# Optimization experiments

Measured on AMD Instinct MI355X. Metric: run time of the kernel, lower is better.

## Reference

```python
import jax, jax.numpy as jnp
import numpy as np

EPS = 1e-7
PI = np.pi


def _vel_to_R(vel):
    # vel: [..., 3] -> rotation matrix [..., 3, 3] (ZY convention from spherical angles)
    rho = jnp.linalg.norm(vel, axis=-1, keepdims=True)
    theta = jnp.arctan2(vel[..., 1:2], vel[..., 0:1])
    theta = theta + (theta < 0).astype(theta.dtype) * (2.0 * PI)  # symmetric_theta=False
    phi = jnp.arccos(jnp.clip(vel[..., 2:3] / (rho + EPS), -1.0, 1.0))
    ct, st = jnp.cos(theta)[..., 0], jnp.sin(theta)[..., 0]
    cp, sp = jnp.cos(phi)[..., 0], jnp.sin(phi)[..., 0]
    z = jnp.zeros_like(ct)
    R = jnp.stack([
        jnp.stack([cp * ct, -st, sp * ct], -1),
        jnp.stack([cp * st, ct, sp * st], -1),
        jnp.stack([-sp, z, cp], -1),
    ], -2)
    return R


def _rotate(R, x):
    return jnp.einsum('...ij,...j->...i', R, x)


def setup_inputs() -> dict:
    key = jax.random.key(0)
    B, N, H, D = 128, 100, 128, 3
    in_size = 2 * D  # 6
    nef = 3 * D + D * (D - 1) // 2 + in_size  # 18 edge features
    ks = jax.random.split(key, 12)

    inputs = jax.random.normal(ks[0], (B, N, in_size), jnp.float32)

    # fully connected edges (no self loops)
    send_np, recv_np = np.nonzero(~np.eye(N, dtype=bool))
    send_edges = jnp.asarray(send_np, jnp.int32)
    recv_edges = jnp.asarray(recv_np, jnp.int32)

    def lin(k, fin, fout):
        return jax.random.normal(k, (fin, fout), jnp.float32) / np.sqrt(fin)

    return dict(
        inputs=inputs,
        W1=lin(ks[1], nef, H), b1=jnp.zeros((H,), jnp.float32),
        W2=lin(ks[2], H, H), b2=jnp.zeros((H,), jnp.float32),
        Wr=lin(ks[3], in_size, H), br=jnp.zeros((H,), jnp.float32),
        W3=lin(ks[4], H, H), b3=jnp.zeros((H,), jnp.float32),
        W4=lin(ks[5], H, H), b4=jnp.zeros((H,), jnp.float32),
        W5=lin(ks[6], H, in_size), b5=jnp.zeros((in_size,), jnp.float32),
        send_edges=send_edges, recv_edges=recv_edges,
    )


def reference(inputs, W1, b1, W2, b2, Wr, br, W3, b3, W4, b4, W5, b5,
              send_edges, recv_edges):
    D = 3
    B, N, _ = inputs.shape

    # ---- Localizer.canonicalize_inputs ----
    vel = inputs[..., D:2 * D]
    Rnode = _vel_to_R(vel)                       # [B,N,3,3]
    Rinv_node = jnp.swapaxes(Rnode, -1, -2)
    canon_vel = _rotate(Rinv_node, vel)
    rel_feat = jnp.concatenate([jnp.zeros_like(canon_vel), canon_vel], -1)  # [B,N,6]

    # ---- Localizer.create_edge_attr ----
    x_j = inputs[:, send_edges]                  # [B,E,6] senders
    x_i = inputs[:, recv_edges]                  # [B,E,6] receivers
    R = _vel_to_R(x_i[..., D:2 * D])
    R_inv = jnp.swapaxes(R, -1, -2)
    rel_pos = x_j[..., :D] - x_i[..., :D]
    rot_rel = _rotate(R_inv, rel_pos)
    send_R = _vel_to_R(x_j[..., D:2 * D])
    rot_or = R_inv @ send_R
    euler = jnp.stack([
        jnp.arctan2(rot_or[..., 1, 0], rot_or[..., 0, 0]),
        jnp.arcsin(-rot_or[..., 2, 0]),
        jnp.arctan2(rot_or[..., 2, 1], rot_or[..., 2, 2]),
    ], -1) / PI
    dist = jnp.linalg.norm(rel_pos, axis=-1, keepdims=True)
    rho_e = jnp.linalg.norm(rot_rel, axis=-1, keepdims=True)
    theta_e = jnp.arctan2(rot_rel[..., 1:2], rot_rel[..., 0:1])  # symmetric theta
    phi_e = jnp.arccos(jnp.clip(rot_rel[..., 2:3] / (rho_e + EPS), -1.0, 1.0))
    rot_vel = _rotate(R_inv, x_j[..., D:2 * D])
    edge_attr = jnp.concatenate(
        [rot_rel, euler, dist, theta_e, phi_e, rot_vel], -1)   # [B,E,12]
    edge_attr = jnp.concatenate([edge_attr, rel_feat[:, recv_edges]], -1)  # [B,E,18]

    # ---- GNN: edge MLP + scatter-mean + out MLP (dropout off in eval) ----
    h = jax.nn.silu(edge_attr @ W1 + b1) @ W2 + b2               # [B,E,H]
    agg = jnp.zeros((B, N, h.shape[-1]), h.dtype).at[:, recv_edges].add(h)
    cnt = jnp.zeros((N,), h.dtype).at[recv_edges].add(1.0)
    agg = agg / jnp.maximum(cnt, 1.0)[None, :, None]             # scatter mean
    aug = agg + rel_feat @ Wr + br
    p = jax.nn.relu(aug @ W3 + b3)
    p = jax.nn.relu(p @ W4 + b4)
    pred = p @ W5 + b5                                           # [B,N,6]

    # ---- Globalizer: rotate each 3-vector chunk back to global frame ----
    gl = jnp.concatenate(
        [_rotate(Rnode, pred[..., i:i + D]) for i in range(0, pred.shape[-1], D)], -1)
    return inputs + gl
```

## Files before the change

kernel.cpp:

```cpp
#include <hip/hip_runtime.h>
#include <math.h>

#define EPSF 1e-7f
constexpr int NN  = 100;
constexpr int DEG = 99;
constexpr int IN  = 6;
constexpr int H   = 128;
constexpr int G   = 4;
constexpr float INV_PI = 0.3183098861837907f;

typedef __attribute__((ext_vector_type(4))) _Float16 half4;
typedef __attribute__((ext_vector_type(8))) _Float16 half8;
typedef __attribute__((ext_vector_type(4))) float f32x4;

constexpr int XST = 144;

__device__ __forceinline__ float clampf(float x, float lo, float hi) {
    return fminf(fmaxf(x, lo), hi);
}
__device__ __forceinline__ float fast_sig(float x) {
    return __builtin_amdgcn_rcpf(1.f + __expf(-x));
}
__device__ __forceinline__ float fast_atan2(float y, float x) {
    float ax = fabsf(x), ay = fabsf(y);
    float mx = fmaxf(ax, ay), mn = fminf(ax, ay);
    float r = mn * __builtin_amdgcn_rcpf(fmaxf(mx, 1e-35f));
    float r2 = r * r;
    float p = fmaf(r2, -0.01172120f, 0.05265332f);
    p = fmaf(r2, p, -0.11643287f);
    p = fmaf(r2, p, 0.19354346f);
    p = fmaf(r2, p, -0.33262347f);
    p = fmaf(r2, p, 0.99997726f);
    float t = r * p;
    t = (ay > ax) ? (1.5707963267948966f - t) : t;
    t = (x < 0.f) ? (3.14159265358979323f - t) : t;
    return copysignf(t, y);
}
__device__ __forceinline__ float fast_asin(float z) {
    return fast_atan2(z, sqrtf(fmaxf(0.f, (1.f - z) * (1.f + z))));
}
__device__ __forceinline__ float fast_acos(float z) {
    return fast_atan2(sqrtf(fmaxf(0.f, (1.f - z) * (1.f + z))), z);
}
__device__ __forceinline__ void vel_to_R(float vx, float vy, float vz, float* R) {
    float rho = sqrtf(vx * vx + vy * vy + vz * vz);
    float rxy = sqrtf(vx * vx + vy * vy);
    float inv = __builtin_amdgcn_rcpf(rxy);
    bool big = rxy > 1e-30f;
    float ct = big ? vx * inv : 1.f;
    float st = big ? vy * inv : 0.f;
    float cp = clampf(vz * __builtin_amdgcn_rcpf(rho + EPSF), -1.f, 1.f);
    float sp = sqrtf(fmaxf(0.f, 1.f - cp * cp));
    R[0] = cp * ct; R[1] = -st; R[2] = sp * ct;
    R[3] = cp * st; R[4] = ct;  R[5] = sp * st;
    R[6] = -sp;     R[7] = 0.f; R[8] = cp;
}

__global__ void conv_w(const float* __restrict__ W1, const float* __restrict__ W2,
                       const float* __restrict__ W3, const float* __restrict__ W4,
                       half4* __restrict__ w1f, half8* __restrict__ wmlp) {
    int t = blockIdx.x * blockDim.x + threadIdx.x;
    if (t >= 104 * 64) return;
    int L = t & 63, f = t >> 6;
    int m = L & 15, qd = L >> 4;
    if (f < 8) {
        int n = f * 16 + m;
        half4 v;
#pragma unroll
        for (int j = 0; j < 4; ++j) {
            int k = qd * 4 + j;
            v[j] = (k < 12) ? (_Float16)W1[k * H + n] : (_Float16)0.f;
        }
        w1f[f * 64 + L] = v;
    } else {
        int ff = f - 8;
        int layer = ff >> 5, rest = ff & 31;
        int kt = rest >> 3, nt = rest & 7;
        const float* W = (layer == 0) ? W2 : (layer == 1) ? W3 : W4;
        int n = nt * 16 + m;
        half8 v;
#pragma unroll
        for (int j = 0; j < 8; ++j)
            v[j] = (_Float16)W[(kt * 32 + qd * 8 + j) * H + n];
        wmlp[((layer * 4 + kt) * 8 + nt) * 64 + L] = v;
    }
}

__global__ __launch_bounds__(128, 6)
void locs_fused(const float* __restrict__ in,
                const float* __restrict__ W1, const float* __restrict__ b1,
                const float* __restrict__ b2,
                const float* __restrict__ Wr, const float* __restrict__ br,
                const float* __restrict__ b3, const float* __restrict__ b4,
                const float* __restrict__ W5, const float* __restrict__ b5,
                const half4* __restrict__ w1f, const half8* __restrict__ wmlp,
                float* __restrict__ out) {
    __shared__ half4 eaA[2 * 7 * 64];
    __shared__ float poolF[1104];
    __shared__ _Float16 xh[G * XST];

    float* baseF = poolF;
    float* xFp   = poolF + 512;
    float* rmFp  = poolF + 1040;
    float* pbF   = poolF;
    float* predF = poolF + 384;

    const int tid = threadIdx.x;
    const int L   = tid & 63;
    const int wv  = tid >> 6;
    const int q   = L >> 4;
    const int lm  = L & 15;
    const int bn0 = blockIdx.x * G;
    const int bB  = bn0 / NN;
    const int n0  = bn0 - bB * NN;

    {
        half4 z = {0, 0, 0, 0};
#pragma unroll
        for (int i = 0; i < 7; ++i) eaA[tid + i * 128] = z;
    }
    if (tid < G) {
        const float* xi = in + (bn0 + tid) * IN;
        float R[9];
        vel_to_R(xi[3], xi[4], xi[5], R);
#pragma unroll
        for (int k = 0; k < 9; ++k) rmFp[tid * 16 + k] = R[k];
        rmFp[tid * 16 + 9]  = R[0] * xi[3] + R[3] * xi[4] + R[6] * xi[5];
        rmFp[tid * 16 + 10] = R[1] * xi[3] + R[4] * xi[4] + R[7] * xi[5];
        rmFp[tid * 16 + 11] = R[2] * xi[3] + R[5] * xi[4] + R[8] * xi[5];
        rmFp[tid * 16 + 12] = xi[0];
        rmFp[tid * 16 + 13] = xi[1];
        rmFp[tid * 16 + 14] = xi[2];
    }
    __syncthreads();

    {
        float w15 = W1[15 * H + tid], w16 = W1[16 * H + tid], w17 = W1[17 * H + tid];
        float b1c = b1[tid];
#pragma unroll
        for (int g = 0; g < G; ++g)
            baseF[g * 128 + tid] = b1c + rmFp[g * 16 + 9] * w15
                                 + rmFp[g * 16 + 10] * w16 + rmFp[g * 16 + 11] * w17;
    }
    half4 bfr[4];
#pragma unroll
    for (int i = 0; i < 4; ++i) bfr[i] = w1f[(wv * 4 + i) * 64 + L];

    auto edge_features = [&](int g, int buf) {
        if (tid < DEG) {
            int nG = n0 + g;
            int s = tid < nG ? tid : tid + 1;
            float Rn[9];
#pragma unroll
            for (int k = 0; k < 9; ++k) Rn[k] = rmFp[g * 16 + k];
            float pix = rmFp[g * 16 + 12], piy = rmFp[g * 16 + 13], piz = rmFp[g * 16 + 14];
            const float* xj = in + (bB * NN + s) * IN;
            float rel0 = xj[0] - pix, rel1 = xj[1] - piy, rel2 = xj[2] - piz;
            float vjx = xj[3], vjy = xj[4], vjz = xj[5];
            float Rs[9];
            vel_to_R(vjx, vjy, vjz, Rs);
            float rr0 = Rn[0] * rel0 + Rn[3] * rel1 + Rn[6] * rel2;
            float rr1 = Rn[1] * rel0 + Rn[4] * rel1 + Rn[7] * rel2;
            float rr2 = Rn[2] * rel0 + Rn[5] * rel1 + Rn[8] * rel2;
            float ro00 = Rn[0] * Rs[0] + Rn[3] * Rs[3] + Rn[6] * Rs[6];
            float ro10 = Rn[1] * Rs[0] + Rn[4] * Rs[3] + Rn[7] * Rs[6];
            float ro20 = Rn[2] * Rs[0] + Rn[5] * Rs[3] + Rn[8] * Rs[6];
            float ro21 = Rn[2] * Rs[1] + Rn[5] * Rs[4] + Rn[8] * Rs[7];
            float ro22 = Rn[2] * Rs[2] + Rn[5] * Rs[5] + Rn[8] * Rs[8];
            float dist = sqrtf(rel0 * rel0 + rel1 * rel1 + rel2 * rel2);
            half4 f0, f1, f2;
            f0[0] = (_Float16)rr0; f0[1] = (_Float16)rr1; f0[2] = (_Float16)rr2;
            f0[3] = (_Float16)(fast_atan2(ro10, ro00) * INV_PI);
            f1[0] = (_Float16)(fast_asin(clampf(-ro20, -1.f, 1.f)) * INV_PI);
            f1[1] = (_Float16)(fast_atan2(ro21, ro22) * INV_PI);
            f1[2] = (_Float16)dist;
            f1[3] = (_Float16)fast_atan2(rr1, rr0);
            f2[0] = (_Float16)fast_acos(clampf(rr2 * __builtin_amdgcn_rcpf(dist + EPSF), -1.f, 1.f));
            f2[1] = (_Float16)(Rn[0] * vjx + Rn[3] * vjy + Rn[6] * vjz);
            f2[2] = (_Float16)(Rn[1] * vjx + Rn[4] * vjy + Rn[7] * vjz);
            f2[3] = (_Float16)(Rn[2] * vjx + Rn[5] * vjy + Rn[8] * vjz);
            int t = tid >> 4, m = tid & 15;
            half4* dst = eaA + buf * 448 + t * 64;
            dst[m]      = f0;
            dst[16 + m] = f1;
            dst[32 + m] = f2;
        }
    };

    edge_features(0, 0);
    __syncthreads();

#pragma unroll
    for (int g = 0; g < G; ++g) {
        float part[4] = {0.f, 0.f, 0.f, 0.f};
        f32x4 c0, c1, c2, c3;
        {
            float bs0 = baseF[g * 128 + wv * 64 +  0 + lm];
            float bs1 = baseF[g * 128 + wv * 64 + 16 + lm];
            float bs2 = baseF[g * 128 + wv * 64 + 32 + lm];
            float bs3 = baseF[g * 128 + wv * 64 + 48 + lm];
            c0 = (f32x4){bs0, bs0, bs0, bs0};
            c1 = (f32x4){bs1, bs1, bs1, bs1};
            c2 = (f32x4){bs2, bs2, bs2, bs2};
            c3 = (f32x4){bs3, bs3, bs3, bs3};
        }
        const half4* ea = eaA + (g & 1) * 448;
#pragma unroll
        for (int t = 0; t < 6; ++t) {
            half4 a = ea[t * 64 + L];
            f32x4 d0 = __builtin_amdgcn_mfma_f32_16x16x16f16(a, bfr[0], c0, 0, 0, 0);
            f32x4 d1 = __builtin_amdgcn_mfma_f32_16x16x16f16(a, bfr[1], c1, 0, 0, 0);
            f32x4 d2 = __builtin_amdgcn_mfma_f32_16x16x16f16(a, bfr[2], c2, 0, 0, 0);
            f32x4 d3 = __builtin_amdgcn_mfma_f32_16x16x16f16(a, bfr[3], c3, 0, 0, 0);
#pragma unroll
            for (int r = 0; r < 4; ++r) {
                part[0] += d0[r] * fast_sig(d0[r]);
                part[1] += d1[r] * fast_sig(d1[r]);
                part[2] += d2[r] * fast_sig(d2[r]);
                part[3] += d3[r] * fast_sig(d3[r]);
            }
        }
        {
            half4 a = ea[6 * 64 + L];
            f32x4 d0 = __builtin_amdgcn_mfma_f32_16x16x16f16(a, bfr[0], c0, 0, 0, 0);
            f32x4 d1 = __builtin_amdgcn_mfma_f32_16x16x16f16(a, bfr[1], c1, 0, 0, 0);
            f32x4 d2 = __builtin_amdgcn_mfma_f32_16x16x16f16(a, bfr[2], c2, 0, 0, 0);
            f32x4 d3 = __builtin_amdgcn_mfma_f32_16x16x16f16(a, bfr[3], c3, 0, 0, 0);
            bool ok = (q == 0);
#pragma unroll
            for (int r = 0; r < 3; ++r) {
                part[0] += ok ? d0[r] * fast_sig(d0[r]) : 0.f;
                part[1] += ok ? d1[r] * fast_sig(d1[r]) : 0.f;
                part[2] += ok ? d2[r] * fast_sig(d2[r]) : 0.f;
                part[3] += ok ? d3[r] * fast_sig(d3[r]) : 0.f;
            }
        }
        if (g < G - 1) edge_features(g + 1, (g + 1) & 1);
#pragma unroll
        for (int i = 0; i < 4; ++i) {
            float v = part[i];
            v += __shfl_xor(v, 16, 64);
            v += __shfl_xor(v, 32, 64);
            if (L < 16) xFp[g * 132 + wv * 64 + i * 16 + L] = v;
        }
        __syncthreads();
    }

#pragma unroll
    for (int layer = 0; layer < 3; ++layer) {
#pragma unroll
        for (int r = 0; r < G; ++r)
            xh[r * XST + tid] = (_Float16)xFp[r * 132 + tid];
        __syncthreads();
        int rowb = (lm & 3) * XST;
        half8 ah[4];
#pragma unroll
        for (int kt = 0; kt < 4; ++kt)
            ah[kt] = *(const half8*)&xh[rowb + kt * 32 + q * 8];
        f32x4 acc[4];
#pragma unroll
        for (int i = 0; i < 4; ++i) acc[i] = (f32x4){0.f, 0.f, 0.f, 0.f};
#pragma unroll
        for (int kt = 0; kt < 4; ++kt) {
            int base = ((layer * 4 + kt) * 8 + wv * 4) * 64 + L;
#pragma unroll
            for (int i = 0; i < 4; ++i) {
                half8 bh = wmlp[base + i * 64];
                acc[i] = __builtin_amdgcn_mfma_f32_16x16x32_f16(ah[kt], bh, acc[i], 0, 0, 0);
            }
        }
        __syncthreads();
        if (L < 16) {
#pragma unroll
            for (int i = 0; i < 4; ++i) {
                int ch = wv * 64 + i * 16 + lm;
                if (layer == 0) {
                    float b2c = b2[ch], brc = br[ch];
                    float w3c = Wr[3 * H + ch], w4c = Wr[4 * H + ch], w5c = Wr[5 * H + ch];
#pragma unroll
                    for (int r = 0; r < 4; ++r)
                        xFp[r * 132 + ch] = acc[i][r] * (1.f / 99.f) + b2c
                                          + rmFp[r * 16 + 9] * w3c + rmFp[r * 16 + 10] * w4c
                                          + rmFp[r * 16 + 11] * w5c + brc;
                } else {
                    float bb = (layer == 1) ? b3[ch] : b4[ch];
#pragma unroll
                    for (int r = 0; r < 4; ++r)
                        xFp[r * 132 + ch] = fmaxf(0.f, acc[i][r] + bb);
                }
            }
        }
        __syncthreads();
    }

    if (tid < 96) {
        int o = tid >> 4, sl = tid & 15, kb = sl * 8;
        float w5[8];
#pragma unroll
        for (int j = 0; j < 8; ++j) w5[j] = W5[(kb + j) * IN + o];
#pragma unroll
        for (int g = 0; g < G; ++g) {
            float s = 0.f;
#pragma unroll
            for (int j = 0; j < 8; ++j) s = fmaf(xFp[g * 132 + kb + j], w5[j], s);
            pbF[g * 96 + sl * 6 + o] = s;
        }
    }
    __syncthreads();
    if (tid < 24) {
        int g = tid / 6, o = tid - g * 6;
        float s = b5[o];
#pragma unroll
        for (int sl = 0; sl < 16; ++sl) s += pbF[g * 96 + sl * 6 + o];
        predF[g * 8 + o] = s;
    }
    __syncthreads();
    if (tid < 24) {
        int g = tid / 6, o = tid - g * 6;
        int r = (o < 3) ? o : o - 3;
        int off = (o < 3) ? 0 : 3;
        float gl = rmFp[g * 16 + r * 3 + 0] * predF[g * 8 + off + 0]
                 + rmFp[g * 16 + r * 3 + 1] * predF[g * 8 + off + 1]
                 + rmFp[g * 16 + r * 3 + 2] * predF[g * 8 + off + 2];
        int bng = bn0 + g;
        out[bng * IN + o] = in[bng * IN + o] + gl;
    }
}

extern "C" void kernel_launch(void* const* d_in, const int* in_sizes, int n_in,
                              void* d_out, int out_size, void* d_ws, size_t ws_size,
                              hipStream_t stream) {
    const float* in = (const float*)d_in[0];
    const float* W1 = (const float*)d_in[1];
    const float* b1 = (const float*)d_in[2];
    const float* W2 = (const float*)d_in[3];
    const float* b2 = (const float*)d_in[4];
    const float* Wr = (const float*)d_in[5];
    const float* br = (const float*)d_in[6];
    const float* W3 = (const float*)d_in[7];
    const float* b3 = (const float*)d_in[8];
    const float* W4 = (const float*)d_in[9];
    const float* b4 = (const float*)d_in[10];
    const float* W5 = (const float*)d_in[11];
    const float* b5 = (const float*)d_in[12];
    float* out = (float*)d_out;

    half4* w1f  = (half4*)d_ws;
    half8* wmlp = (half8*)((char*)d_ws + 4096);

    const int BN = in_sizes[0] / IN;
    conv_w<<<26, 256, 0, stream>>>(W1, W2, W3, W4, w1f, wmlp);
    locs_fused<<<BN / G, 128, 0, stream>>>(in, W1, b1, b2, Wr, br, b3, b4,
                                           W5, b5, w1f, wmlp, out);
}
```

Baseline: 147.2 us.

## Precompute per-batch node rotations in LDS and drop masked tail SiLU handling

Each block now computes rotation matrices for all 100 nodes of its batch once into shared memory, so per-edge code reads the sender rotation instead of recomputing vel_to_R (atan2/acos/sin/cos) per edge. The last MFMA tile is processed unmasked like the others, and the contribution of the 13 padded zero rows (whose pre-activation equals the bias) is subtracted analytically. SiLU evaluation is batched so all exps are issued before the reciprocals. Launch bounds no longer request 6 blocks per CU. The cost is extra redundant per-block work (100 rotations per block of 4 nodes), more LDS, and possible occupancy changes.

```diff
diff --git a/kernel.cpp b/kernel.cpp
--- a/kernel.cpp
+++ b/kernel.cpp
@@ -86,7 +86,7 @@
     }
 }
 
-__global__ __launch_bounds__(128, 6)
+__global__ __launch_bounds__(128)
 void locs_fused(const float* __restrict__ in,
                 const float* __restrict__ W1, const float* __restrict__ b1,
                 const float* __restrict__ b2,
@@ -96,19 +96,19 @@
                 const half4* __restrict__ w1f, const half8* __restrict__ wmlp,
                 float* __restrict__ out) {
     __shared__ half4 eaA[2 * 7 * 64];
-    __shared__ float poolF[1104];
+    __shared__ float sR[NN * 16];
+    __shared__ float poolF[1056];
     __shared__ _Float16 xh[G * XST];
 
     float* baseF = poolF;
     float* xFp   = poolF + 512;
-    float* rmFp  = poolF + 1040;
+    float* cvF   = poolF + 1040;
     float* pbF   = poolF;
     float* predF = poolF + 384;
 
     const int tid = threadIdx.x;
     const int L   = tid & 63;
     const int wv  = tid >> 6;
-    const int q   = L >> 4;
     const int lm  = L & 15;
     const int bn0 = blockIdx.x * G;
     const int bB  = bn0 / NN;
@@ -119,18 +119,24 @@
 #pragma unroll
         for (int i = 0; i < 7; ++i) eaA[tid + i * 128] = z;
     }
-    if (tid < G) {
-        const float* xi = in + (bn0 + tid) * IN;
+    if (tid < NN) {
+        const float* xi = in + (bB * NN + tid) * IN;
         float R[9];
         vel_to_R(xi[3], xi[4], xi[5], R);
-#pragma unroll
-        for (int k = 0; k < 9; ++k) rmFp[tid * 16 + k] = R[k];
-        rmFp[tid * 16 + 9]  = R[0] * xi[3] + R[3] * xi[4] + R[6] * xi[5];
-        rmFp[tid * 16 + 10] = R[1] * xi[3] + R[4] * xi[4] + R[7] * xi[5];
-        rmFp[tid * 16 + 11] = R[2] * xi[3] + R[5] * xi[4] + R[8] * xi[5];
-        rmFp[tid * 16 + 12] = xi[0];
-        rmFp[tid * 16 + 13] = xi[1];
-        rmFp[tid * 16 + 14] = xi[2];
+        float* dst = sR + tid * 16;
+#pragma unroll
+        for (int k = 0; k < 9; ++k) dst[k] = R[k];
+        dst[9]  = xi[3]; dst[10] = xi[4]; dst[11] = xi[5];
+        dst[12] = xi[0]; dst[13] = xi[1]; dst[14] = xi[2];
+        dst[15] = 0.f;
+    }
+    __syncthreads();
+    if (tid < G) {
+        const float* rg = sR + (n0 + tid) * 16;
+        float vx = rg[9], vy = rg[10], vz = rg[11];
+        cvF[tid * 4 + 0] = rg[0] * vx + rg[3] * vy + rg[6] * vz;
+        cvF[tid * 4 + 1] = rg[1] * vx + rg[4] * vy + rg[7] * vz;
+        cvF[tid * 4 + 2] = rg[2] * vx + rg[5] * vy + rg[8] * vz;
     }
     __syncthreads();
 
@@ -139,8 +145,8 @@
         float b1c = b1[tid];
 #pragma unroll
         for (int g = 0; g < G; ++g)
-            baseF[g * 128 + tid] = b1c + rmFp[g * 16 + 9] * w15
-                                 + rmFp[g * 16 + 10] * w16 + rmFp[g * 16 + 11] * w17;
+            baseF[g * 128 + tid] = b1c + cvF[g * 4 + 0] * w15
+                                 + cvF[g * 4 + 1] * w16 + cvF[g * 4 + 2] * w17;
     }
     half4 bfr[4];
 #pragma unroll
@@ -150,23 +156,21 @@
         if (tid < DEG) {
             int nG = n0 + g;
             int s = tid < nG ? tid : tid + 1;
+            const float* rn = sR + nG * 16;
+            const float* rs = sR + s * 16;
             float Rn[9];
 #pragma unroll
-            for (int k = 0; k < 9; ++k) Rn[k] = rmFp[g * 16 + k];
-            float pix = rmFp[g * 16 + 12], piy = rmFp[g * 16 + 13], piz = rmFp[g * 16 + 14];
-            const float* xj = in + (bB * NN + s) * IN;
-            float rel0 = xj[0] - pix, rel1 = xj[1] - piy, rel2 = xj[2] - piz;
-            float vjx = xj[3], vjy = xj[4], vjz = xj[5];
-            float Rs[9];
-            vel_to_R(vjx, vjy, vjz, Rs);
+            for (int k = 0; k < 9; ++k) Rn[k] = rn[k];
+            float rel0 = rs[12] - rn[12], rel1 = rs[13] - rn[13], rel2 = rs[14] - rn[14];
+            float vjx = rs[9], vjy = rs[10], vjz = rs[11];
             float rr0 = Rn[0] * rel0 + Rn[3] * rel1 + Rn[6] * rel2;
             float rr1 = Rn[1] * rel0 + Rn[4] * rel1 + Rn[7] * rel2;
             float rr2 = Rn[2] * rel0 + Rn[5] * rel1 + Rn[8] * rel2;
-            float ro00 = Rn[0] * Rs[0] + Rn[3] * Rs[3] + Rn[6] * Rs[6];
-            float ro10 = Rn[1] * Rs[0] + Rn[4] * Rs[3] + Rn[7] * Rs[6];
-            float ro20 = Rn[2] * Rs[0] + Rn[5] * Rs[3] + Rn[8] * Rs[6];
-            float ro21 = Rn[2] * Rs[1] + Rn[5] * Rs[4] + Rn[8] * Rs[7];
-            float ro22 = Rn[2] * Rs[2] + Rn[5] * Rs[5] + Rn[8] * Rs[8];
+            float ro00 = Rn[0] * rs[0] + Rn[3] * rs[3] + Rn[6] * rs[6];
+            float ro10 = Rn[1] * rs[0] + Rn[4] * rs[3] + Rn[7] * rs[6];
+            float ro20 = Rn[2] * rs[0] + Rn[5] * rs[3] + Rn[8] * rs[6];
+            float ro21 = Rn[2] * rs[1] + Rn[5] * rs[4] + Rn[8] * rs[7];
+            float ro22 = Rn[2] * rs[2] + Rn[5] * rs[5] + Rn[8] * rs[8];
             float dist = sqrtf(rel0 * rel0 + rel1 * rel1 + rel2 * rel2);
             half4 f0, f1, f2;
             f0[0] = (_Float16)rr0; f0[1] = (_Float16)rr1; f0[2] = (_Float16)rr2;
@@ -193,47 +197,31 @@
 #pragma unroll
     for (int g = 0; g < G; ++g) {
         float part[4] = {0.f, 0.f, 0.f, 0.f};
-        f32x4 c0, c1, c2, c3;
-        {
-            float bs0 = baseF[g * 128 + wv * 64 +  0 + lm];
-            float bs1 = baseF[g * 128 + wv * 64 + 16 + lm];
-            float bs2 = baseF[g * 128 + wv * 64 + 32 + lm];
-            float bs3 = baseF[g * 128 + wv * 64 + 48 + lm];
-            c0 = (f32x4){bs0, bs0, bs0, bs0};
-            c1 = (f32x4){bs1, bs1, bs1, bs1};
-            c2 = (f32x4){bs2, bs2, bs2, bs2};
-            c3 = (f32x4){bs3, bs3, bs3, bs3};
+        float bs[4];
+        f32x4 c[4];
+#pragma unroll
+        for (int i = 0; i < 4; ++i) {
+            bs[i] = baseF[g * 128 + wv * 64 + i * 16 + lm];
+            c[i] = (f32x4){bs[i], bs[i], bs[i], bs[i]};
         }
         const half4* ea = eaA + (g & 1) * 448;
 #pragma unroll
-        for (int t = 0; t < 6; ++t) {
+        for (int t = 0; t < 7; ++t) {
             half4 a = ea[t * 64 + L];
-            f32x4 d0 = __builtin_amdgcn_mfma_f32_16x16x16f16(a, bfr[0], c0, 0, 0, 0);
-            f32x4 d1 = __builtin_amdgcn_mfma_f32_16x16x16f16(a, bfr[1], c1, 0, 0, 0);
-            f32x4 d2 = __builtin_amdgcn_mfma_f32_16x16x16f16(a, bfr[2], c2, 0, 0, 0);
-            f32x4 d3 = __builtin_amdgcn_mfma_f32_16x16x16f16(a, bfr[3], c3, 0, 0, 0);
+            f32x4 d0 = __builtin_amdgcn_mfma_f32_16x16x16f16(a, bfr[0], c[0], 0, 0, 0);
+            f32x4 d1 = __builtin_amdgcn_mfma_f32_16x16x16f16(a, bfr[1], c[1], 0, 0, 0);
+            f32x4 d2 = __builtin_amdgcn_mfma_f32_16x16x16f16(a, bfr[2], c[2], 0, 0, 0);
+            f32x4 d3 = __builtin_amdgcn_mfma_f32_16x16x16f16(a, bfr[3], c[3], 0, 0, 0);
+            float dv[16], ev[16];
 #pragma unroll
             for (int r = 0; r < 4; ++r) {
-                part[0] += d0[r] * fast_sig(d0[r]);
-                part[1] += d1[r] * fast_sig(d1[r]);
-                part[2] += d2[r] * fast_sig(d2[r]);
-                part[3] += d3[r] * fast_sig(d3[r]);
+                dv[r] = d0[r]; dv[4 + r] = d1[r]; dv[8 + r] = d2[r]; dv[12 + r] = d3[r];
             }
-        }
-        {
-            half4 a = ea[6 * 64 + L];
-            f32x4 d0 = __builtin_amdgcn_mfma_f32_16x16x16f16(a, bfr[0], c0, 0, 0, 0);
-            f32x4 d1 = __builtin_amdgcn_mfma_f32_16x16x16f16(a, bfr[1], c1, 0, 0, 0);
-            f32x4 d2 = __builtin_amdgcn_mfma_f32_16x16x16f16(a, bfr[2], c2, 0, 0, 0);
-            f32x4 d3 = __builtin_amdgcn_mfma_f32_16x16x16f16(a, bfr[3], c3, 0, 0, 0);
-            bool ok = (q == 0);
-#pragma unroll
-            for (int r = 0; r < 3; ++r) {
-                part[0] += ok ? d0[r] * fast_sig(d0[r]) : 0.f;
-                part[1] += ok ? d1[r] * fast_sig(d1[r]) : 0.f;
-                part[2] += ok ? d2[r] * fast_sig(d2[r]) : 0.f;
-                part[3] += ok ? d3[r] * fast_sig(d3[r]) : 0.f;
-            }
+#pragma unroll
+            for (int j = 0; j < 16; ++j) ev[j] = __expf(-dv[j]);
+#pragma unroll
+            for (int j = 0; j < 16; ++j)
+                part[j >> 2] += dv[j] * __builtin_amdgcn_rcpf(1.f + ev[j]);
         }
         if (g < G - 1) edge_features(g + 1, (g + 1) & 1);
 #pragma unroll
@@ -241,11 +229,13 @@
             float v = part[i];
             v += __shfl_xor(v, 16, 64);
             v += __shfl_xor(v, 32, 64);
-            if (L < 16) xFp[g * 132 + wv * 64 + i * 16 + L] = v;
+            if (L < 16)
+                xFp[g * 132 + wv * 64 + i * 16 + L] = v - 13.f * bs[i] * fast_sig(bs[i]);
         }
         __syncthreads();
     }
 
+    const int q = L >> 4;
 #pragma unroll
     for (int layer = 0; layer < 3; ++layer) {
 #pragma unroll
@@ -280,8 +270,8 @@
 #pragma unroll
                     for (int r = 0; r < 4; ++r)
                         xFp[r * 132 + ch] = acc[i][r] * (1.f / 99.f) + b2c
-                                          + rmFp[r * 16 + 9] * w3c + rmFp[r * 16 + 10] * w4c
-                                          + rmFp[r * 16 + 11] * w5c + brc;
+                                          + cvF[r * 4 + 0] * w3c + cvF[r * 4 + 1] * w4c
+                                          + cvF[r * 4 + 2] * w5c + brc;
                 } else {
                     float bb = (layer == 1) ? b3[ch] : b4[ch];
 #pragma unroll
@@ -319,9 +309,10 @@
         int g = tid / 6, o = tid - g * 6;
         int r = (o < 3) ? o : o - 3;
         int off = (o < 3) ? 0 : 3;
-        float gl = rmFp[g * 16 + r * 3 + 0] * predF[g * 8 + off + 0]
-                 + rmFp[g * 16 + r * 3 + 1] * predF[g * 8 + off + 1]
-                 + rmFp[g * 16 + r * 3 + 2] * predF[g * 8 + off + 2];
+        const float* Rg = sR + (n0 + g) * 16;
+        float gl = Rg[r * 3 + 0] * predF[g * 8 + off + 0]
+                 + Rg[r * 3 + 1] * predF[g * 8 + off + 1]
+                 + Rg[r * 3 + 2] * predF[g * 8 + off + 2];
         int bng = bn0 + g;
         out[bng * IN + o] = in[bng * IN + o] + gl;
     }
```

Result: slower. 163.1 us (+10.8%).
